# Kernel tuning notes

Measured on AMD Instinct MI355X. Metric: run time of the kernel, lower is better.

## Reference

```python
import jax, jax.numpy as jnp
import numpy as np

N = 100000
E = 1600000
IN_FEATS = 512
N_CLASSES = 40
H1, D1 = 8, 8
H2, D2 = 1, N_CLASSES


def gat_conv(x, src, dst, W, al, ar, b, H, D):
    # x: [N, F] -> h: [N, H, D]
    n = x.shape[0]
    h = (x @ W).reshape(n, H, D)
    el = (h * al[None]).sum(-1)  # [N, H]
    er = (h * ar[None]).sum(-1)  # [N, H]
    e = jax.nn.leaky_relu(el[src] + er[dst], 0.2)  # [E, H]
    # segment softmax over destination neighborhoods
    emax = jax.ops.segment_max(e, dst, num_segments=n)  # [N, H]
    ee = jnp.exp(e - emax[dst])
    denom = jax.ops.segment_sum(ee, dst, num_segments=n)  # [N, H]
    a = ee / (denom[dst] + 1e-9)  # [E, H]
    m = h[src] * a[:, :, None]  # [E, H, D]
    out = jax.ops.segment_sum(m, dst, num_segments=n)  # [N, H, D]
    return out + b.reshape(1, H, D)


def setup_inputs() -> dict:
    key = jax.random.key(0)
    ks = jax.random.split(key, 12)
    g1 = 1.0 / np.sqrt(IN_FEATS)
    g2 = 1.0 / np.sqrt(H1 * D1)
    return {
        "x": jax.random.normal(ks[0], (N, IN_FEATS), jnp.float32),
        "src": jax.random.randint(ks[1], (E,), 0, N, jnp.int32),
        "dst": jax.random.randint(ks[2], (E,), 0, N, jnp.int32),
        "W1": jax.random.normal(ks[3], (IN_FEATS, H1 * D1), jnp.float32) * g1,
        "al1": jax.random.normal(ks[4], (H1, D1), jnp.float32) * 0.1,
        "ar1": jax.random.normal(ks[5], (H1, D1), jnp.float32) * 0.1,
        "b1": jnp.zeros((H1 * D1,), jnp.float32),
        "W2": jax.random.normal(ks[6], (H1 * D1, H2 * D2), jnp.float32) * g2,
        "al2": jax.random.normal(ks[7], (H2, D2), jnp.float32) * 0.1,
        "ar2": jax.random.normal(ks[8], (H2, D2), jnp.float32) * 0.1,
        "b2": jnp.zeros((H2 * D2,), jnp.float32),
    }


def reference(x, src, dst, W1, al1, ar1, b1, W2, al2, ar2, b2):
    h = gat_conv(x, src, dst, W1, al1, ar1, b1, H1, D1)  # [N, 8, 8]
    h = jax.nn.elu(h.reshape(N, H1 * D1))  # [N, 64]
    h = gat_conv(h, src, dst, W2, al2, ar2, b2, H2, D2).mean(axis=1)  # [N, n_classes]
    return jax.nn.log_softmax(h, axis=1)
```

## Files before the change

### kernel.cpp

```cpp
#include <hip/hip_runtime.h>
#include <hip/hip_bf16.h>
#include <math.h>

#define NCLS 40
#define H2S 64
#define PWG 256
#define BSH 9
#define NBMAX 512
#define SRCB 23
#define CSRCAP 14336

typedef __attribute__((ext_vector_type(8))) short bf16x8;
typedef __attribute__((ext_vector_type(4))) float f32x4;

__device__ inline float bf2f(ushort u) {
    unsigned v = ((unsigned)u) << 16;
    float f;
    __builtin_memcpy(&f, &v, 4);
    return f;
}
__device__ inline ushort f2bf(float f) {
    unsigned v;
    __builtin_memcpy(&v, &f, 4);
    unsigned r = (v + 0x7FFFu + ((v >> 16) & 1u)) >> 16;
    return (ushort)r;
}
__device__ inline unsigned pkbf(float a, float b) {
    unsigned ua, ub;
    __builtin_memcpy(&ua, &a, 4);
    __builtin_memcpy(&ub, &b, 4);
    return __builtin_amdgcn_perm(ub + 0x8000u, ua + 0x8000u, 0x07060302u);
}

__global__ __launch_bounds__(256) void hist_prep_kernel(
    const int* __restrict__ dst, int* __restrict__ hist, int Ee, int chunk, int NB,
    const float* __restrict__ W1, ushort* __restrict__ W1t,
    const float* __restrict__ W2, const float* __restrict__ al2,
    const float* __restrict__ ar2, float* __restrict__ wal2,
    float* __restrict__ war2)
{
    if (blockIdx.x >= PWG) {
        int bb = blockIdx.x - PWG;
        if (bb < 128) {
            int id = bb * 256 + threadIdx.x;
            int k = id >> 6, c = id & 63;
            W1t[c * 512 + k] = f2bf(W1[k * 64 + c]);
        } else if (threadIdx.x < 64) {
            int k = threadIdx.x;
            float a = 0.f, b = 0.f;
            for (int c = 0; c < NCLS; c++) {
                float w = W2[k * NCLS + c];
                a += w * al2[c];
                b += w * ar2[c];
            }
            wal2[k] = a;
            war2[k] = b;
        }
        return;
    }
    __shared__ int lh[NBMAX];
    const int wg = blockIdx.x, tid = threadIdx.x;
    for (int i = tid; i < NB; i += 256) lh[i] = 0;
    __syncthreads();
    const int beg = wg * chunk;
    const int endv = min(Ee, beg + chunk);
    for (int i = beg + tid; i < endv; i += 256) atomicAdd(&lh[dst[i] >> BSH], 1);
    __syncthreads();
    for (int b = tid; b < NB; b += 256) hist[b * PWG + wg] = lh[b];
}

__global__ __launch_bounds__(256) void scanA_kernel(int* __restrict__ hist,
                                                    int* __restrict__ bucketTot)
{
    __shared__ int s[256];
    const int b = blockIdx.x, tid = threadIdx.x;
    int v = hist[b * PWG + tid];
    s[tid] = v;
    __syncthreads();
#pragma unroll
    for (int o = 1; o < 256; o <<= 1) {
        int t = (tid >= o) ? s[tid - o] : 0;
        __syncthreads();
        s[tid] += t;
        __syncthreads();
    }
    hist[b * PWG + tid] = s[tid] - v;
    if (tid == 255) bucketTot[b] = s[255];
}

__global__ __launch_bounds__(256) void part_gemm1_kernel(
    const int* __restrict__ src, const int* __restrict__ dst,
    const int* __restrict__ hist, const int* __restrict__ bucketTot,
    unsigned* __restrict__ ebuf, int Ee, int chunk, int NB,
    const float* __restrict__ x, const ushort* __restrict__ W1t,
    const float* __restrict__ al1, const float* __restrict__ ar1,
    ushort* __restrict__ h1b, float* __restrict__ el1,
    float* __restrict__ er1, int Nn)
{
    __shared__ ushort As[64 * 72];
    __shared__ ushort Bs[64 * 72];

    if (blockIdx.x < PWG) {
        int* cur = (int*)As;
        int* stmp = (int*)Bs;
        const int wg = blockIdx.x, tid = threadIdx.x;
        int v = (tid < NB) ? bucketTot[tid] : 0;
        stmp[tid] = v;
        __syncthreads();
#pragma unroll
        for (int o = 1; o < 256; o <<= 1) {
            int t = (tid >= o) ? stmp[tid - o] : 0;
            __syncthreads();
            stmp[tid] += t;
            __syncthreads();
        }
        if (tid < NB) cur[tid] = hist[tid * PWG + wg] + (stmp[tid] - v);
        __syncthreads();
        const int beg = wg * chunk;
        const int endv = min(Ee, beg + chunk);
        for (int i = beg + tid; i < endv; i += 256) {
            int d = dst[i];
            int p = atomicAdd(&cur[d >> BSH], 1);
            ebuf[p] = ((unsigned)(d & ((1 << BSH) - 1)) << SRCB) | (unsigned)src[i];
        }
        return;
    }

    const int t = threadIdx.x;
    const int lane = t & 63, w = t >> 6;
    const int tile = (blockIdx.x - PWG) * 64;

    f32x4 acc[4] = {};

    const int sr = t >> 2;
    const int sk = (t & 3) * 16;
    const int arow = tile + sr;
    const bool rowok = arow < Nn;
    const float* xrow = x + (size_t)arow * 512;
    const ushort* wrow = W1t + (size_t)sr * 512;

    const int r = lane & 15, g = lane >> 4;

    float4 f0 = make_float4(0.f, 0.f, 0.f, 0.f), f1 = f0, f2 = f0, f3 = f0;
    bf16x8 bv0, bv1;
    if (rowok) {
        f0 = *(const float4*)(xrow + sk);
        f1 = *(const float4*)(xrow + sk + 4);
        f2 = *(const float4*)(xrow + sk + 8);
        f3 = *(const float4*)(xrow + sk + 12);
    }
    bv0 = *(const bf16x8*)(wrow + sk);
    bv1 = *(const bf16x8*)(wrow + sk + 8);

    for (int k0 = 0; k0 < 512; k0 += 64) {
        uint4 aw0, aw1;
        aw0.x = pkbf(f0.x, f0.y); aw0.y = pkbf(f0.z, f0.w);
        aw0.z = pkbf(f1.x, f1.y); aw0.w = pkbf(f1.z, f1.w);
        aw1.x = pkbf(f2.x, f2.y); aw1.y = pkbf(f2.z, f2.w);
        aw1.z = pkbf(f3.x, f3.y); aw1.w = pkbf(f3.z, f3.w);
        *(uint4*)&As[sr * 72 + sk] = aw0;
        *(uint4*)&As[sr * 72 + sk + 8] = aw1;
        *(bf16x8*)&Bs[sr * 72 + sk] = bv0;
        *(bf16x8*)&Bs[sr * 72 + sk + 8] = bv1;
        __syncthreads();

        int k1 = k0 + 64;
        if (k1 < 512) {
            if (rowok) {
                f0 = *(const float4*)(xrow + k1 + sk);
                f1 = *(const float4*)(xrow + k1 + sk + 4);
                f2 = *(const float4*)(xrow + k1 + sk + 8);
                f3 = *(const float4*)(xrow + k1 + sk + 12);
            }
            bv0 = *(const bf16x8*)(wrow + k1 + sk);
            bv1 = *(const bf16x8*)(wrow + k1 + sk + 8);
        }

        bf16x8 af0 = *(const bf16x8*)&As[(w * 16 + r) * 72 + g * 8];
        bf16x8 af1 = *(const bf16x8*)&As[(w * 16 + r) * 72 + 32 + g * 8];
#pragma unroll
        for (int cb = 0; cb < 4; cb++) {
            bf16x8 bf0 = *(const bf16x8*)&Bs[(cb * 16 + r) * 72 + g * 8];
            acc[cb] = __builtin_amdgcn_mfma_f32_16x16x32_bf16(af0, bf0, acc[cb], 0, 0, 0);
        }
#pragma unroll
        for (int cb = 0; cb < 4; cb++) {
            bf16x8 bf1 = *(const bf16x8*)&Bs[(cb * 16 + r) * 72 + 32 + g * 8];
            acc[cb] = __builtin_amdgcn_mfma_f32_16x16x32_bf16(af1, bf1, acc[cb], 0, 0, 0);
        }
        __syncthreads();
    }

    float alv[4], arv[4];
#pragma unroll
    for (int cb = 0; cb < 4; cb++) {
        alv[cb] = al1[cb * 16 + r];
        arv[cb] = ar1[cb * 16 + r];
    }
#pragma unroll
    for (int v = 0; v < 4; v++) {
        int row = tile + w * 16 + g * 4 + v;
        bool ok = row < Nn;
#pragma unroll
        for (int cb = 0; cb < 4; cb++) {
            if (ok) h1b[(size_t)row * 64 + cb * 16 + r] = f2bf(acc[cb][v]);
            float pel = acc[cb][v] * alv[cb];
            float per = acc[cb][v] * arv[cb];
            pel += __shfl_xor(pel, 1); per += __shfl_xor(per, 1);
            pel += __shfl_xor(pel, 2); per += __shfl_xor(per, 2);
            pel += __shfl_xor(pel, 4); per += __shfl_xor(per, 4);
            if (ok && (r & 7) == 0) {
                int head = cb * 2 + (r >> 3);
                el1[row * 8 + head] = pel;
                er1[row * 8 + head] = per;
            }
        }
    }
}

__global__ __launch_bounds__(512) void bucket_csr_kernel(const unsigned* __restrict__ ebuf,
                                                         const int* __restrict__ bucketTot,
                                                         int* __restrict__ row_start,
                                                         int* __restrict__ perm_src,
                                                         int Nn, int Ee, int NB)
{
    __shared__ unsigned stage[CSRCAP];
    __shared__ int cnt[512];
    __shared__ int s[512];
    __shared__ int cur[512];
    __shared__ int bt[256];
    const int b = blockIdx.x, tid = threadIdx.x;
    const int base = b << BSH;

    if (tid < 256) bt[tid] = (tid < NB) ? bucketTot[tid] : 0;
    __syncthreads();
#pragma unroll
    for (int o = 1; o < 256; o <<= 1) {
        int t = (tid >= o && tid < 256) ? bt[tid - o] : 0;
        __syncthreads();
        if (tid < 256) bt[tid] += t;
        __syncthreads();
    }
    const int be = bt[b];
    const int bb = be - bucketTot[b];
    const int m = be - bb;

    cnt[tid] = 0;
    __syncthreads();
    for (int idx = tid; idx < m; idx += 512) {
        unsigned pk = ebuf[bb + idx];
        if (idx < CSRCAP) stage[idx] = pk;
        atomicAdd(&cnt[pk >> SRCB], 1);
    }
    __syncthreads();
    int v = cnt[tid];
    s[tid] = v;
    __syncthreads();
#pragma unroll
    for (int o = 1; o < 512; o <<= 1) {
        int t = (tid >= o) ? s[tid - o] : 0;
        __syncthreads();
        s[tid] += t;
        __syncthreads();
    }
    const int off = bb + s[tid] - v;
    const int node = base + tid;
    if (node < Nn) row_start[node] = off;
    cur[tid] = off;
    __syncthreads();
    for (int idx = tid; idx < m; idx += 512) {
        unsigned pk = (idx < CSRCAP) ? stage[idx] : ebuf[bb + idx];
        int p = atomicAdd(&cur[pk >> SRCB], 1);
        perm_src[p] = (int)(pk & ((1u << SRCB) - 1u));
    }
    if (b == NB - 1 && tid == 0) row_start[Nn] = Ee;
}

__global__ __launch_bounds__(256) void agg1_kernel(
    const ushort* __restrict__ h1b, const float* __restrict__ el1,
    const float* __restrict__ er1, const int* __restrict__ row_start,
    const int* __restrict__ perm_src, const float* __restrict__ b1,
    ushort* __restrict__ hmidb, int Nn)
{
    const int wid = (blockIdx.x * blockDim.x + threadIdx.x) >> 6;
    const int lane = threadIdx.x & 63;
    if (wid >= Nn) return;
    const int g = lane >> 4;
    const int q = lane & 15;
    const int h = q >> 1;
    const int beg = row_start[wid], end = row_start[wid + 1];
    const float er = er1[wid * 8 + h];

    float a0 = 0.f, a1 = 0.f, a2 = 0.f, a3 = 0.f, denom = 0.f;
    for (int i0 = beg; i0 < end; i0 += 64) {
        const int cnt = min(end - i0, 64);
        int pv = (i0 + lane < end) ? perm_src[i0 + lane] : 0;
        for (int j = 0; j < cnt; j += 8) {
            const int e0 = j + g, e1 = j + 4 + g;
            const int s0 = __shfl(pv, min(e0, cnt - 1));
            const int s1 = __shfl(pv, min(e1, cnt - 1));
            ushort4 r0 = *(const ushort4*)&h1b[(size_t)s0 * 64 + q * 4];
            ushort4 r1 = *(const ushort4*)&h1b[(size_t)s1 * 64 + q * 4];
            float x0 = el1[s0 * 8 + h];
            float x1 = el1[s1 * 8 + h];
            float e = x0 + er;
            e = (e >= 0.f) ? e : 0.2f * e;
            float w0 = (e0 < cnt) ? __expf(e) : 0.f;
            e = x1 + er;
            e = (e >= 0.f) ? e : 0.2f * e;
            float w1 = (e1 < cnt) ? __expf(e) : 0.f;
            denom += w0 + w1;
            a0 += bf2f(r0.x) * w0 + bf2f(r1.x) * w1;
            a1 += bf2f(r0.y) * w0 + bf2f(r1.y) * w1;
            a2 += bf2f(r0.z) * w0 + bf2f(r1.z) * w1;
            a3 += bf2f(r0.w) * w0 + bf2f(r1.w) * w1;
        }
    }
    denom += __shfl_xor(denom, 16); denom += __shfl_xor(denom, 32);
    a0 += __shfl_xor(a0, 16); a0 += __shfl_xor(a0, 32);
    a1 += __shfl_xor(a1, 16); a1 += __shfl_xor(a1, 32);
    a2 += __shfl_xor(a2, 16); a2 += __shfl_xor(a2, 32);
    a3 += __shfl_xor(a3, 16); a3 += __shfl_xor(a3, 32);
    if (g == 0) {
        const float4 bv = *(const float4*)&b1[q * 4];
        const float inv = 1.f / (denom + 1e-9f);
        float v0 = a0 * inv + bv.x;
        float v1 = a1 * inv + bv.y;
        float v2 = a2 * inv + bv.z;
        float v3 = a3 * inv + bv.w;
        v0 = (v0 > 0.f) ? v0 : expm1f(v0);
        v1 = (v1 > 0.f) ? v1 : expm1f(v1);
        v2 = (v2 > 0.f) ? v2 : expm1f(v2);
        v3 = (v3 > 0.f) ? v3 : expm1f(v3);
        uint2 o;
        o.x = pkbf(v0, v1);
        o.y = pkbf(v2, v3);
        *(uint2*)&hmidb[(size_t)wid * 64 + q * 4] = o;
    }
}

__global__ __launch_bounds__(256) void gemm2_kernel(
    const ushort* __restrict__ hmidb, const float* __restrict__ W2,
    const float* __restrict__ wal2, const float* __restrict__ war2,
    ushort* __restrict__ h2b, int Nn)
{
    __shared__ float w2s[64 * NCLS];
    __shared__ float wals[64], wars[64];
    for (int i = threadIdx.x; i < 64 * NCLS; i += blockDim.x) w2s[i] = W2[i];
    if (threadIdx.x < 64) {
        wals[threadIdx.x] = wal2[threadIdx.x];
        wars[threadIdx.x] = war2[threadIdx.x];
    }
    __syncthreads();
    int n = blockIdx.x * blockDim.x + threadIdx.x;
    if (n >= Nn) return;

    float out[NCLS];
#pragma unroll
    for (int c = 0; c < NCLS; c++) out[c] = 0.f;
    float accel = 0.f, accer = 0.f;

#pragma unroll 4
    for (int k4 = 0; k4 < 16; k4++) {
        ushort4 u = *(const ushort4*)&hmidb[(size_t)n * 64 + k4 * 4];
        float h0 = bf2f(u.x), h1 = bf2f(u.y), h2 = bf2f(u.z), h3 = bf2f(u.w);
        accel += h0 * wals[k4 * 4] + h1 * wals[k4 * 4 + 1] + h2 * wals[k4 * 4 + 2] + h3 * wals[k4 * 4 + 3];
        accer += h0 * wars[k4 * 4] + h1 * wars[k4 * 4 + 1] + h2 * wars[k4 * 4 + 2] + h3 * wars[k4 * 4 + 3];
#pragma unroll
        for (int c = 0; c < NCLS; c++) {
            out[c] += h0 * w2s[(k4 * 4 + 0) * NCLS + c] + h1 * w2s[(k4 * 4 + 1) * NCLS + c] +
                      h2 * w2s[(k4 * 4 + 2) * NCLS + c] + h3 * w2s[(k4 * 4 + 3) * NCLS + c];
        }
    }
    ushort* row = h2b + (size_t)n * H2S;
#pragma unroll
    for (int c = 0; c < NCLS; c += 2) {
        *(unsigned*)&row[c] = pkbf(out[c], out[c + 1]);
    }
    ((float*)row)[20] = accel;
    ((float*)row)[21] = accer;
}

__global__ __launch_bounds__(256) void agg2_kernel(
    const ushort* __restrict__ h2b, const int* __restrict__ row_start,
    const int* __restrict__ perm_src, const float* __restrict__ b2,
    float* __restrict__ out, int Nn)
{
    const int wid = (blockIdx.x * blockDim.x + threadIdx.x) >> 6;
    const int lane = threadIdx.x & 63;
    if (wid >= Nn) return;
    const int g = lane >> 4;
    const int q = lane & 15;
    const int beg = row_start[wid], end = row_start[wid + 1];
    const float er = ((const float*)(h2b + (size_t)wid * H2S))[21];

    float a0 = 0.f, a1 = 0.f, a2 = 0.f, a3 = 0.f, denom = 0.f;
    for (int i0 = beg; i0 < end; i0 += 64) {
        const int cnt = min(end - i0, 64);
        int pv = (i0 + lane < end) ? perm_src[i0 + lane] : 0;
        for (int j = 0; j < cnt; j += 8) {
            const int e0 = j + g, e1 = j + 4 + g;
            const int s0 = __shfl(pv, min(e0, cnt - 1));
            const int s1 = __shfl(pv, min(e1, cnt - 1));
            const ushort* rp0 = h2b + (size_t)s0 * H2S;
            const ushort* rp1 = h2b + (size_t)s1 * H2S;
            ushort4 r0 = *(const ushort4*)(rp0 + q * 4);
            ushort4 r1 = *(const ushort4*)(rp1 + q * 4);
            float x0 = ((const float*)rp0)[20];
            float x1 = ((const float*)rp1)[20];
            float e = x0 + er;
            e = (e >= 0.f) ? e : 0.2f * e;
            float w0 = (e0 < cnt) ? __expf(e) : 0.f;
            e = x1 + er;
            e = (e >= 0.f) ? e : 0.2f * e;
            float w1 = (e1 < cnt) ? __expf(e) : 0.f;
            denom += w0 + w1;
            a0 += bf2f(r0.x) * w0 + bf2f(r1.x) * w1;
            a1 += bf2f(r0.y) * w0 + bf2f(r1.y) * w1;
            a2 += bf2f(r0.z) * w0 + bf2f(r1.z) * w1;
            a3 += bf2f(r0.w) * w0 + bf2f(r1.w) * w1;
        }
    }
    denom += __shfl_xor(denom, 16); denom += __shfl_xor(denom, 32);
    a0 += __shfl_xor(a0, 16); a0 += __shfl_xor(a0, 32);
    a1 += __shfl_xor(a1, 16); a1 += __shfl_xor(a1, 32);
    a2 += __shfl_xor(a2, 16); a2 += __shfl_xor(a2, 32);
    a3 += __shfl_xor(a3, 16); a3 += __shfl_xor(a3, 32);

    const bool act = (g == 0) && (q < 10);
    float v0, v1, v2, v3;
    if (act) {
        const float4 bv = *(const float4*)&b2[q * 4];
        const float inv = 1.f / (denom + 1e-9f);
        v0 = a0 * inv + bv.x;
        v1 = a1 * inv + bv.y;
        v2 = a2 * inv + bv.z;
        v3 = a3 * inv + bv.w;
    } else {
        v0 = v1 = v2 = v3 = -1e30f;
    }
    float mx = fmaxf(fmaxf(v0, v1), fmaxf(v2, v3));
#pragma unroll
    for (int o = 1; o < 64; o <<= 1) mx = fmaxf(mx, __shfl_xor(mx, o));
    float sx = act ? (__expf(v0 - mx) + __expf(v1 - mx) + __expf(v2 - mx) + __expf(v3 - mx)) : 0.f;
#pragma unroll
    for (int o = 1; o < 64; o <<= 1) sx += __shfl_xor(sx, o);
    if (act) {
        float lg = mx + __logf(sx);
        float4 o4 = make_float4(v0 - lg, v1 - lg, v2 - lg, v3 - lg);
        *(float4*)&out[(size_t)wid * NCLS + q * 4] = o4;
    }
}

extern "C" void kernel_launch(void* const* d_in, const int* in_sizes, int n_in,
                              void* d_out, int out_size, void* d_ws, size_t ws_size,
                              hipStream_t stream)
{
    const float* x   = (const float*)d_in[0];
    const int*   src = (const int*)d_in[1];
    const int*   dst = (const int*)d_in[2];
    const float* W1  = (const float*)d_in[3];
    const float* al1 = (const float*)d_in[4];
    const float* ar1 = (const float*)d_in[5];
    const float* b1  = (const float*)d_in[6];
    const float* W2  = (const float*)d_in[7];
    const float* al2 = (const float*)d_in[8];
    const float* ar2 = (const float*)d_in[9];
    const float* b2  = (const float*)d_in[10];
    float* out = (float*)d_out;

    const int Nn = in_sizes[0] / 512;
    const int Ee = in_sizes[1];
    const int NB = (Nn + (1 << BSH) - 1) >> BSH;
    const int chunk = (Ee + PWG - 1) / PWG;

    char* wsb = (char*)d_ws;
    size_t off = 0;
    auto alloc = [&](size_t bytes) -> void* {
        off = (off + 15) & ~(size_t)15;
        void* p = wsb + off;
        off += bytes;
        return p;
    };
    ushort* h1b   = (ushort*)alloc((size_t)Nn * 64 * 2);
    ushort* hmidb = (ushort*)alloc((size_t)Nn * 64 * 2);
    ushort* h2b   = (ushort*)alloc((size_t)Nn * H2S * 2);
    ushort* W1t   = (ushort*)alloc(64 * 512 * 2);
    float* el1  = (float*)alloc((size_t)Nn * 8 * 4);
    float* er1  = (float*)alloc((size_t)Nn * 8 * 4);
    float* wal2 = (float*)alloc(64 * 4);
    float* war2 = (float*)alloc(64 * 4);
    int* row_start  = (int*)alloc((size_t)(Nn + 1) * 4);
    int* hist       = (int*)alloc((size_t)NB * PWG * 4);
    int* bucketTot  = (int*)alloc((size_t)NB * 4);
    int* perm_src   = (int*)alloc((size_t)Ee * 4);
    unsigned* ebuf  = (unsigned*)alloc((size_t)Ee * 4);

    hist_prep_kernel<<<PWG + 129, 256, 0, stream>>>(dst, hist, Ee, chunk, NB,
                                                    W1, W1t, W2, al2, ar2, wal2, war2);
    scanA_kernel<<<NB, 256, 0, stream>>>(hist, bucketTot);
    part_gemm1_kernel<<<PWG + (Nn + 63) / 64, 256, 0, stream>>>(
        src, dst, hist, bucketTot, ebuf, Ee, chunk, NB,
        x, W1t, al1, ar1, h1b, el1, er1, Nn);
    bucket_csr_kernel<<<NB, 512, 0, stream>>>(ebuf, bucketTot, row_start, perm_src, Nn, Ee, NB);

    agg1_kernel<<<(Nn + 3) / 4, 256, 0, stream>>>(h1b, el1, er1, row_start, perm_src, b1, hmidb, Nn);

    gemm2_kernel<<<(Nn + 255) / 256, 256, 0, stream>>>(hmidb, W2, wal2, war2, h2b, Nn);
    agg2_kernel<<<(Nn + 3) / 4, 256, 0, stream>>>(h2b, row_start, perm_src, b2, out, Nn);
}
```

Measured before the change: 225.9 us.

## Drop scan kernel by recomputing bucket offsets; widen GEMM1 tile to 128 rows

Removes the separate scanA kernel launch. Partition workgroups and bucket_csr blocks now each re-sum the transposed histogram (256x256 ints) to get bucket totals and per-workgroup prefixes. This trades one launch and its dependency for redundant reads of the histogram. Separately, the GEMM1 tile doubles to 128 rows per block with two accumulator sets per wave, reusing each B tile in LDS twice and halving the GEMM block count, at the cost of more registers and LDS.

```diff
diff --git a/kernel.cpp b/kernel.cpp
--- a/kernel.cpp
+++ b/kernel.cpp
@@ -6,7 +6,6 @@
 #define H2S 64
 #define PWG 256
 #define BSH 9
-#define NBMAX 512
 #define SRCB 23
 #define CSRCAP 14336
 
@@ -58,63 +57,50 @@
         }
         return;
     }
-    __shared__ int lh[NBMAX];
+    __shared__ int lh[256];
     const int wg = blockIdx.x, tid = threadIdx.x;
-    for (int i = tid; i < NB; i += 256) lh[i] = 0;
+    lh[tid] = 0;
     __syncthreads();
     const int beg = wg * chunk;
     const int endv = min(Ee, beg + chunk);
     for (int i = beg + tid; i < endv; i += 256) atomicAdd(&lh[dst[i] >> BSH], 1);
     __syncthreads();
-    for (int b = tid; b < NB; b += 256) hist[b * PWG + wg] = lh[b];
-}
-
-__global__ __launch_bounds__(256) void scanA_kernel(int* __restrict__ hist,
-                                                    int* __restrict__ bucketTot)
-{
-    __shared__ int s[256];
-    const int b = blockIdx.x, tid = threadIdx.x;
-    int v = hist[b * PWG + tid];
-    s[tid] = v;
-    __syncthreads();
-#pragma unroll
-    for (int o = 1; o < 256; o <<= 1) {
-        int t = (tid >= o) ? s[tid - o] : 0;
-        __syncthreads();
-        s[tid] += t;
-        __syncthreads();
-    }
-    hist[b * PWG + tid] = s[tid] - v;
-    if (tid == 255) bucketTot[b] = s[255];
+    if (tid < NB) hist[wg * 256 + tid] = lh[tid];
 }
 
 __global__ __launch_bounds__(256) void part_gemm1_kernel(
     const int* __restrict__ src, const int* __restrict__ dst,
-    const int* __restrict__ hist, const int* __restrict__ bucketTot,
-    unsigned* __restrict__ ebuf, int Ee, int chunk, int NB,
+    const int* __restrict__ hist, unsigned* __restrict__ ebuf,
+    int Ee, int chunk, int NB,
     const float* __restrict__ x, const ushort* __restrict__ W1t,
     const float* __restrict__ al1, const float* __restrict__ ar1,
     ushort* __restrict__ h1b, float* __restrict__ el1,
     float* __restrict__ er1, int Nn)
 {
-    __shared__ ushort As[64 * 72];
+    __shared__ ushort As[128 * 72];
     __shared__ ushort Bs[64 * 72];
 
     if (blockIdx.x < PWG) {
         int* cur = (int*)As;
-        int* stmp = (int*)Bs;
+        int* stmp = cur + 256;
         const int wg = blockIdx.x, tid = threadIdx.x;
-        int v = (tid < NB) ? bucketTot[tid] : 0;
-        stmp[tid] = v;
+        int partial = 0, total = 0;
+#pragma unroll 4
+        for (int wp = 0; wp < PWG; wp++) {
+            int v = (tid < NB) ? hist[wp * 256 + tid] : 0;
+            total += v;
+            if (wp < wg) partial += v;
+        }
+        stmp[tid] = total;
         __syncthreads();
 #pragma unroll
         for (int o = 1; o < 256; o <<= 1) {
-            int t = (tid >= o) ? stmp[tid - o] : 0;
+            int tv = (tid >= o) ? stmp[tid - o] : 0;
             __syncthreads();
-            stmp[tid] += t;
+            stmp[tid] += tv;
             __syncthreads();
         }
-        if (tid < NB) cur[tid] = hist[tid * PWG + wg] + (stmp[tid] - v);
+        cur[tid] = (stmp[tid] - total) + partial;
         __syncthreads();
         const int beg = wg * chunk;
         const int endv = min(Ee, beg + chunk);
@@ -128,65 +114,74 @@
 
     const int t = threadIdx.x;
     const int lane = t & 63, w = t >> 6;
-    const int tile = (blockIdx.x - PWG) * 64;
-
-    f32x4 acc[4] = {};
-
-    const int sr = t >> 2;
-    const int sk = (t & 3) * 16;
+    const int tile = (blockIdx.x - PWG) * 128;
+
+    f32x4 acc[2][4] = {};
+
+    const int sr = t >> 1;
+    const int skA = (t & 1) * 32;
+    const int sc = t >> 2;
+    const int skB = (t & 3) * 16;
     const int arow = tile + sr;
     const bool rowok = arow < Nn;
     const float* xrow = x + (size_t)arow * 512;
-    const ushort* wrow = W1t + (size_t)sr * 512;
+    const ushort* wrow = W1t + (size_t)sc * 512;
 
     const int r = lane & 15, g = lane >> 4;
 
-    float4 f0 = make_float4(0.f, 0.f, 0.f, 0.f), f1 = f0, f2 = f0, f3 = f0;
+    float4 fa[8];
+#pragma unroll
+    for (int i = 0; i < 8; i++) fa[i] = make_float4(0.f, 0.f, 0.f, 0.f);
     bf16x8 bv0, bv1;
     if (rowok) {
-        f0 = *(const float4*)(xrow + sk);
-        f1 = *(const float4*)(xrow + sk + 4);
-        f2 = *(const float4*)(xrow + sk + 8);
-        f3 = *(const float4*)(xrow + sk + 12);
-    }
-    bv0 = *(const bf16x8*)(wrow + sk);
-    bv1 = *(const bf16x8*)(wrow + sk + 8);
+#pragma unroll
+        for (int i = 0; i < 8; i++) fa[i] = *(const float4*)(xrow + skA + i * 4);
+    }
+    bv0 = *(const bf16x8*)(wrow + skB);
+    bv1 = *(const bf16x8*)(wrow + skB + 8);
 
     for (int k0 = 0; k0 < 512; k0 += 64) {
-        uint4 aw0, aw1;
-        aw0.x = pkbf(f0.x, f0.y); aw0.y = pkbf(f0.z, f0.w);
-        aw0.z = pkbf(f1.x, f1.y); aw0.w = pkbf(f1.z, f1.w);
-        aw1.x = pkbf(f2.x, f2.y); aw1.y = pkbf(f2.z, f2.w);
-        aw1.z = pkbf(f3.x, f3.y); aw1.w = pkbf(f3.z, f3.w);
-        *(uint4*)&As[sr * 72 + sk] = aw0;
-        *(uint4*)&As[sr * 72 + sk + 8] = aw1;
-        *(bf16x8*)&Bs[sr * 72 + sk] = bv0;
-        *(bf16x8*)&Bs[sr * 72 + sk + 8] = bv1;
+        uint4 q0, q1;
+        q0.x = pkbf(fa[0].x, fa[0].y); q0.y = pkbf(fa[0].z, fa[0].w);
+        q0.z = pkbf(fa[1].x, fa[1].y); q0.w = pkbf(fa[1].z, fa[1].w);
+        q1.x = pkbf(fa[2].x, fa[2].y); q1.y = pkbf(fa[2].z, fa[2].w);
+        q1.z = pkbf(fa[3].x, fa[3].y); q1.w = pkbf(fa[3].z, fa[3].w);
+        *(uint4*)&As[sr * 72 + skA] = q0;
+        *(uint4*)&As[sr * 72 + skA + 8] = q1;
+        q0.x = pkbf(fa[4].x, fa[4].y); q0.y = pkbf(fa[4].z, fa[4].w);
+        q0.z = pkbf(fa[5].x, fa[5].y); q0.w = pkbf(fa[5].z, fa[5].w);
+        q1.x = pkbf(fa[6].x, fa[6].y); q1.y = pkbf(fa[6].z, fa[6].w);
+        q1.z = pkbf(fa[7].x, fa[7].y); q1.w = pkbf(fa[7].z, fa[7].w);
+        *(uint4*)&As[sr * 72 + skA + 16] = q0;
+        *(uint4*)&As[sr * 72 + skA + 24] = q1;
+        *(bf16x8*)&Bs[sc * 72 + skB] = bv0;
+        *(bf16x8*)&Bs[sc * 72 + skB + 8] = bv1;
         __syncthreads();
 
         int k1 = k0 + 64;
         if (k1 < 512) {
             if (rowok) {
-                f0 = *(const float4*)(xrow + k1 + sk);
-                f1 = *(const float4*)(xrow + k1 + sk + 4);
-                f2 = *(const float4*)(xrow + k1 + sk + 8);
-                f3 = *(const float4*)(xrow + k1 + sk + 12);
+#pragma unroll
+                for (int i = 0; i < 8; i++) fa[i] = *(const float4*)(xrow + k1 + skA + i * 4);
             }
-            bv0 = *(const bf16x8*)(wrow + k1 + sk);
-            bv1 = *(const bf16x8*)(wrow + k1 + sk + 8);
-        }
-
-        bf16x8 af0 = *(const bf16x8*)&As[(w * 16 + r) * 72 + g * 8];
-        bf16x8 af1 = *(const bf16x8*)&As[(w * 16 + r) * 72 + 32 + g * 8];
-#pragma unroll
-        for (int cb = 0; cb < 4; cb++) {
-            bf16x8 bf0 = *(const bf16x8*)&Bs[(cb * 16 + r) * 72 + g * 8];
-            acc[cb] = __builtin_amdgcn_mfma_f32_16x16x32_bf16(af0, bf0, acc[cb], 0, 0, 0);
-        }
-#pragma unroll
-        for (int cb = 0; cb < 4; cb++) {
-            bf16x8 bf1 = *(const bf16x8*)&Bs[(cb * 16 + r) * 72 + 32 + g * 8];
-            acc[cb] = __builtin_amdgcn_mfma_f32_16x16x32_bf16(af1, bf1, acc[cb], 0, 0, 0);
+            bv0 = *(const bf16x8*)(wrow + k1 + skB);
+            bv1 = *(const bf16x8*)(wrow + k1 + skB + 8);
+        }
+
+#pragma unroll
+        for (int m = 0; m < 2; m++) {
+            bf16x8 af0 = *(const bf16x8*)&As[(w * 32 + m * 16 + r) * 72 + g * 8];
+            bf16x8 af1 = *(const bf16x8*)&As[(w * 32 + m * 16 + r) * 72 + 32 + g * 8];
+#pragma unroll
+            for (int cb = 0; cb < 4; cb++) {
+                bf16x8 bf0 = *(const bf16x8*)&Bs[(cb * 16 + r) * 72 + g * 8];
+                acc[m][cb] = __builtin_amdgcn_mfma_f32_16x16x32_bf16(af0, bf0, acc[m][cb], 0, 0, 0);
+            }
+#pragma unroll
+            for (int cb = 0; cb < 4; cb++) {
+                bf16x8 bf1 = *(const bf16x8*)&Bs[(cb * 16 + r) * 72 + 32 + g * 8];
+                acc[m][cb] = __builtin_amdgcn_mfma_f32_16x16x32_bf16(af1, bf1, acc[m][cb], 0, 0, 0);
+            }
         }
         __syncthreads();
     }
@@ -198,28 +193,31 @@
         arv[cb] = ar1[cb * 16 + r];
     }
 #pragma unroll
-    for (int v = 0; v < 4; v++) {
-        int row = tile + w * 16 + g * 4 + v;
-        bool ok = row < Nn;
-#pragma unroll
-        for (int cb = 0; cb < 4; cb++) {
-            if (ok) h1b[(size_t)row * 64 + cb * 16 + r] = f2bf(acc[cb][v]);
-            float pel = acc[cb][v] * alv[cb];
-            float per = acc[cb][v] * arv[cb];
-            pel += __shfl_xor(pel, 1); per += __shfl_xor(per, 1);
-            pel += __shfl_xor(pel, 2); per += __shfl_xor(per, 2);
-            pel += __shfl_xor(pel, 4); per += __shfl_xor(per, 4);
-            if (ok && (r & 7) == 0) {
-                int head = cb * 2 + (r >> 3);
-                el1[row * 8 + head] = pel;
-                er1[row * 8 + head] = per;
+    for (int m = 0; m < 2; m++) {
+#pragma unroll
+        for (int v = 0; v < 4; v++) {
+            int row = tile + w * 32 + m * 16 + g * 4 + v;
+            bool ok = row < Nn;
+#pragma unroll
+            for (int cb = 0; cb < 4; cb++) {
+                if (ok) h1b[(size_t)row * 64 + cb * 16 + r] = f2bf(acc[m][cb][v]);
+                float pel = acc[m][cb][v] * alv[cb];
+                float per = acc[m][cb][v] * arv[cb];
+                pel += __shfl_xor(pel, 1); per += __shfl_xor(per, 1);
+                pel += __shfl_xor(pel, 2); per += __shfl_xor(per, 2);
+                pel += __shfl_xor(pel, 4); per += __shfl_xor(per, 4);
+                if (ok && (r & 7) == 0) {
+                    int head = cb * 2 + (r >> 3);
+                    el1[row * 8 + head] = pel;
+                    er1[row * 8 + head] = per;
+                }
             }
         }
     }
 }
 
 __global__ __launch_bounds__(512) void bucket_csr_kernel(const unsigned* __restrict__ ebuf,
-                                                         const int* __restrict__ bucketTot,
+                                                         const int* __restrict__ hist,
                                                          int* __restrict__ row_start,
                                                          int* __restrict__ perm_src,
                                                          int Nn, int Ee, int NB)
@@ -232,17 +230,22 @@
     const int b = blockIdx.x, tid = threadIdx.x;
     const int base = b << BSH;
 
-    if (tid < 256) bt[tid] = (tid < NB) ? bucketTot[tid] : 0;
+    if (tid < 256) {
+        int tot = 0;
+#pragma unroll 4
+        for (int wp = 0; wp < PWG; wp++) tot += (tid < NB) ? hist[wp * 256 + tid] : 0;
+        bt[tid] = tot;
+    }
     __syncthreads();
 #pragma unroll
     for (int o = 1; o < 256; o <<= 1) {
-        int t = (tid >= o && tid < 256) ? bt[tid - o] : 0;
-        __syncthreads();
-        if (tid < 256) bt[tid] += t;
+        int tv = (tid < 256 && tid >= o) ? bt[tid - o] : 0;
+        __syncthreads();
+        if (tid < 256) bt[tid] += tv;
         __syncthreads();
     }
     const int be = bt[b];
-    const int bb = be - bucketTot[b];
+    const int bb = (b == 0) ? 0 : bt[b - 1];
     const int m = be - bb;
 
     cnt[tid] = 0;
@@ -491,18 +494,16 @@
     float* wal2 = (float*)alloc(64 * 4);
     float* war2 = (float*)alloc(64 * 4);
     int* row_start  = (int*)alloc((size_t)(Nn + 1) * 4);
-    int* hist       = (int*)alloc((size_t)NB * PWG * 4);
-    int* bucketTot  = (int*)alloc((size_t)NB * 4);
+    int* hist       = (int*)alloc((size_t)PWG * 256 * 4);
     int* perm_src   = (int*)alloc((size_t)Ee * 4);
     unsigned* ebuf  = (unsigned*)alloc((size_t)Ee * 4);
 
     hist_prep_kernel<<<PWG + 129, 256, 0, stream>>>(dst, hist, Ee, chunk, NB,
                                                     W1, W1t, W2, al2, ar2, wal2, war2);
-    scanA_kernel<<<NB, 256, 0, stream>>>(hist, bucketTot);
-    part_gemm1_kernel<<<PWG + (Nn + 63) / 64, 256, 0, stream>>>(
-        src, dst, hist, bucketTot, ebuf, Ee, chunk, NB,
+    part_gemm1_kernel<<<PWG + (Nn + 127) / 128, 256, 0, stream>>>(
+        src, dst, hist, ebuf, Ee, chunk, NB,
         x, W1t, al1, ar1, h1b, el1, er1, Nn);
-    bucket_csr_kernel<<<NB, 512, 0, stream>>>(ebuf, bucketTot, row_start, perm_src, Nn, Ee, NB);
+    bucket_csr_kernel<<<NB, 512, 0, stream>>>(ebuf, hist, row_start, perm_src, Nn, Ee, NB);
 
     agg1_kernel<<<(Nn + 3) / 4, 256, 0, stream>>>(h1b, el1, er1, row_start, perm_src, b1, hmidb, Nn);
 
```

Result: slower. 257.4 us (+13.9%).
